# Kernel tuning notes

Measured on AMD Instinct MI355X. Metric: run time of the kernel, lower is better.

The kernel has to match this reference:

```python
import jax, jax.numpy as jnp
import numpy as np

B, N, E, D, L, NC = 48, 96, 1024, 300, 4, 7
NEG = 1e30


def _gru(x, h, w_ih, w_hh, b_ih, b_hh):
    # torch.nn.GRUCell math; weights are (3D, D) in torch layout
    gi = x @ w_ih.T + b_ih
    gh = h @ w_hh.T + b_hh
    ir, iz, inn = jnp.split(gi, 3, axis=-1)
    hr, hz, hn = jnp.split(gh, 3, axis=-1)
    r = jax.nn.sigmoid(ir + hr)
    z = jax.nn.sigmoid(iz + hz)
    n = jnp.tanh(inn + r * hn)
    return (1.0 - z) * n + z * h


def _layer(Cin, Hin, adj, cwi, cwh, cbi, cbh, pwi, pwh, pbi, pbh, wq, wk, gb):
    b, n, d = Cin.shape
    zeros = jnp.zeros((b, d), Cin.dtype)
    c0 = _gru(Cin[:, 0], zeros, cwi, cwh, cbi, cbh)          # GRUCell with h=0
    p0 = _gru(zeros, Cin[:, 0], pwi, pwh, pbi, pbh)          # M=0 at step 0
    P0 = jnp.zeros_like(Cin).at[:, 0].set(p0)                # growing P kept as full buffer
    pos = jnp.arange(n)

    def step(P, i):
        q = Cin[:, i]                                        # (B, D)
        mask = adj[:, i] * (pos < i).astype(adj.dtype)       # only predecessors j < i
        # GatLinear: Linear(cat(Q,K)) == Q.wq + K.wk + b
        alpha = (q @ wq)[:, None] + P @ wk + gb              # (B, N)
        alpha = alpha - (1.0 - mask) * NEG                   # mask_logic
        w = jax.nn.softmax(alpha, axis=-1)
        M = jnp.einsum('bn,bnd->bd', w, P)
        c_i = _gru(q, M, cwi, cwh, cbi, cbh)
        p_i = _gru(M, Hin[:, i], pwi, pwh, pbi, pbh)
        P = jax.lax.dynamic_update_slice(P, p_i[:, None, :], (0, i, 0))
        return P, c_i

    P, Cs = jax.lax.scan(step, P0, jnp.arange(1, n))
    CL = jnp.concatenate([c0[:, None], jnp.moveaxis(Cs, 0, 1)], axis=1)  # (B, N, D)
    return CL, P


def reference(features, adj, s_mask, fc1_w, fc1_b,
              gc_wih, gc_whh, gc_bih, gc_bhh,
              gp_wih, gp_whh, gp_bih, gp_bhh,
              gat_wq, gat_wk, gat_b,
              mlp_w0, mlp_b0, mlp_w1, mlp_b1, mlp_w2, mlp_b2):
    # s_mask is unused when no_rel_attn=True (faithful to torch forward)
    H0 = jax.nn.relu(features @ fc1_w + fc1_b)
    H_list = [H0]
    C_list = [H0]
    for l in range(L):
        CL, P = _layer(C_list[l], H_list[l], adj,
                       gc_wih[l], gc_whh[l], gc_bih[l], gc_bhh[l],
                       gp_wih[l], gp_whh[l], gp_bih[l], gp_bhh[l],
                       gat_wq[l], gat_wk[l], gat_b[l])
        C_list.append(CL)
        H_list.append(CL)
        H_list.append(P)
    H_list.append(features)
    H = jnp.concatenate(H_list, axis=2)                      # (B, N, 9D + E)
    x = jax.nn.relu(H @ mlp_w0 + mlp_b0)
    x = jax.nn.relu(x @ mlp_w1 + mlp_b1)
    logits = x @ mlp_w2 + mlp_b2                             # (B, N, NC)
    return logits


def setup_inputs() -> dict:
    key = jax.random.key(0)
    ks = jax.random.split(key, 25)
    s = 0.02

    def p(k, shape):
        return jax.random.normal(k, shape, jnp.float32) * s

    features = jax.random.normal(ks[0], (B, N, E), jnp.float32)
    # DAG adjacency: random predecessors, strictly lower-triangular, previous
    # utterance always connected (guarantees a nonempty attention context)
    base = jax.random.bernoulli(ks[1], 0.5, (B, N, N)).astype(jnp.float32)
    tri = jnp.tril(jnp.ones((N, N), jnp.float32), -1)
    prev = jnp.eye(N, k=-1, dtype=jnp.float32)
    adj = jnp.maximum(base * tri, prev[None])
    s_mask = jax.random.randint(ks[2], (B, N, N), 0, 2, jnp.int32)
    in_dim = D * (2 * L + 1) + E
    return {
        'features': features, 'adj': adj, 's_mask': s_mask,
        'fc1_w': p(ks[3], (E, D)), 'fc1_b': p(ks[4], (D,)),
        'gc_wih': p(ks[5], (L, 3 * D, D)), 'gc_whh': p(ks[6], (L, 3 * D, D)),
        'gc_bih': p(ks[7], (L, 3 * D)), 'gc_bhh': p(ks[8], (L, 3 * D)),
        'gp_wih': p(ks[9], (L, 3 * D, D)), 'gp_whh': p(ks[10], (L, 3 * D, D)),
        'gp_bih': p(ks[11], (L, 3 * D)), 'gp_bhh': p(ks[12], (L, 3 * D)),
        'gat_wq': p(ks[13], (L, D)), 'gat_wk': p(ks[14], (L, D)), 'gat_b': p(ks[15], (L,)),
        'mlp_w0': p(ks[16], (in_dim, D)), 'mlp_b0': p(ks[17], (D,)),
        'mlp_w1': p(ks[18], (D, D)), 'mlp_b1': p(ks[19], (D,)),
        'mlp_w2': p(ks[20], (D, NC)), 'mlp_b2': p(ks[21], (NC,)),
    }
```

## Files before the change

### kernel.cpp

```cpp
#include <hip/hip_runtime.h>
#include <math.h>

#define BB 48
#define NN 96
#define EE 1024
#define DD 300
#define LL 4
#define G3 900
#define PP 150
#define PP2 152
#define NC4 38
#define HDIM 3724
#define ROWS (BB*NN)
#define NEGI -1.0e30f
#define KP300 304
#define GIC_TILES 540

typedef _Float16 half2_t __attribute__((ext_vector_type(2)));
typedef _Float16 h8 __attribute__((ext_vector_type(8)));
typedef float f4 __attribute__((ext_vector_type(4)));

__device__ __forceinline__ float sigm(float x){ return 1.0f/(1.0f+expf(-x)); }

__device__ __forceinline__ void dot4(const h8 wv, const h8 mc,
                                     float& a0, float& a1, float& a2, float& a3)
{
    half2_t w0,w1,w2,w3,m0,m1,m2,m3;
    w0.x=wv[0]; w0.y=wv[1]; m0.x=mc[0]; m0.y=mc[1];
    w1.x=wv[2]; w1.y=wv[3]; m1.x=mc[2]; m1.y=mc[3];
    w2.x=wv[4]; w2.y=wv[5]; m2.x=mc[4]; m2.y=mc[5];
    w3.x=wv[6]; w3.y=wv[7]; m3.x=mc[6]; m3.y=mc[7];
    a0 = __builtin_amdgcn_fdot2(w0, m0, a0, false);
    a1 = __builtin_amdgcn_fdot2(w1, m1, a1, false);
    a2 = __builtin_amdgcn_fdot2(w2, m2, a2, false);
    a3 = __builtin_amdgcn_fdot2(w3, m3, a3, false);
}

__global__ __launch_bounds__(256) void pack_w_q(const float* __restrict__ src_all,
                                                h8* __restrict__ dst)
{
    int l = blockIdx.y;
    int idx = blockIdx.x*256 + threadIdx.x;
    if (idx >= NC4*G3) return;
    int c = idx / G3, gate = idx % G3;
    const float* src = src_all + (size_t)l*G3*DD + (size_t)gate*DD;
    h8 v;
    #pragma unroll
    for (int j=0;j<8;j++){
        int d = 8*c + j;
        v[j] = (d<DD) ? (_Float16)src[d] : (_Float16)0.f;
    }
    dst[(size_t)l*NC4*G3 + idx] = v;
}

__global__ __launch_bounds__(256) void conv_gru_w(const float* __restrict__ gp_whh,
                                                  const float* __restrict__ gc_wih,
                                                  const float* __restrict__ gc_whh,
                                                  _Float16* __restrict__ outp)
{
    int z = blockIdx.y; int l = z/3, wsel = z%3;
    const float* src = (wsel==0?gp_whh:wsel==1?gc_wih:gc_whh) + (size_t)l*G3*DD;
    _Float16* dst = outp + (size_t)z*G3*KP300;
    int idx = blockIdx.x*256 + threadIdx.x;
    if (idx >= G3*KP300) return;
    int n = idx/KP300, k = idx%KP300;
    dst[idx] = (k<DD) ? (_Float16)src[(size_t)n*DD+k] : (_Float16)0.f;
}

__global__ __launch_bounds__(256) void convT(const float* __restrict__ src,
                                             _Float16* __restrict__ dst,
                                             int K, int N, int Kpad)
{
    int idx = blockIdx.x*256 + threadIdx.x;
    if (idx >= N*Kpad) return;
    int n = idx/Kpad, k = idx%Kpad;
    dst[idx] = (k<K) ? (_Float16)src[(size_t)k*N + n] : (_Float16)0.f;
}

__device__ __forceinline__ void gemm_tile(
    int m0, int n0, int tid,
    const float* __restrict__ A, int lda,
    const _Float16* __restrict__ B, int Kpad,
    const float* __restrict__ bias,
    float* __restrict__ C, int ldc,
    int N, int K, int relu)
{
    constexpr int KPS=40;
    __shared__ _Float16 As[128][KPS];
    __shared__ _Float16 Bs[64][KPS];
    int w = tid>>6, lane = tid&63;
    int wy = w>>1, wx = w&1;
    int lm = lane&15, q = lane>>4;

    f4 acc[4][2];
    #pragma unroll
    for (int a=0;a<4;a++)
        #pragma unroll
        for (int b=0;b<2;b++)
            #pragma unroll
            for (int r=0;r<4;r++) acc[a][b][r]=0.f;

    int am = tid>>1, akg = (tid&1)*16;
    int bn = tid>>2, bkg = (tid&3)*8;
    const float* arow = A + (size_t)(m0+am)*lda;

    for (int k0=0; k0<K; k0+=32){
        {
            __align__(16) _Float16 av[16];
            #pragma unroll
            for (int u=0;u<16;u+=4){
                int k = k0 + akg + u;
                float x0,x1,x2,x3;
                if (k+4 <= K){
                    float4 v = *(const float4*)(arow + k);
                    x0=v.x;x1=v.y;x2=v.z;x3=v.w;
                } else {
                    x0 = (k  <K)? arow[k  ]:0.f;
                    x1 = (k+1<K)? arow[k+1]:0.f;
                    x2 = (k+2<K)? arow[k+2]:0.f;
                    x3 = (k+3<K)? arow[k+3]:0.f;
                }
                av[u]=(_Float16)x0; av[u+1]=(_Float16)x1;
                av[u+2]=(_Float16)x2; av[u+3]=(_Float16)x3;
            }
            *(h8*)&As[am][akg]   = *(h8*)&av[0];
            *(h8*)&As[am][akg+8] = *(h8*)&av[8];
        }
        {
            int gk = k0 + bkg;
            h8 bv;
            #pragma unroll
            for (int j=0;j<8;j++) bv[j]=(_Float16)0.f;
            if (n0+bn < N && gk < Kpad)
                bv = *(const h8*)(B + (size_t)(n0+bn)*Kpad + gk);
            *(h8*)&Bs[bn][bkg] = bv;
        }
        __syncthreads();
        h8 af[4], bf[2];
        #pragma unroll
        for (int mb=0; mb<4; mb++) af[mb] = *(h8*)&As[wy*64+mb*16+lm][q*8];
        #pragma unroll
        for (int nb=0; nb<2; nb++) bf[nb] = *(h8*)&Bs[wx*32+nb*16+lm][q*8];
        #pragma unroll
        for (int mb=0; mb<4; mb++)
            #pragma unroll
            for (int nb=0; nb<2; nb++)
                acc[mb][nb] = __builtin_amdgcn_mfma_f32_16x16x32_f16(af[mb], bf[nb], acc[mb][nb], 0,0,0);
        __syncthreads();
    }
    #pragma unroll
    for (int mb=0; mb<4; mb++){
        int r0 = m0 + wy*64 + mb*16 + q*4;
        #pragma unroll
        for (int nb=0; nb<2; nb++){
            int c = n0 + wx*32 + nb*16 + lm;
            if (c < N){
                float bb = bias[c];
                #pragma unroll
                for (int reg=0; reg<4; reg++){
                    float v = acc[mb][nb][reg] + bb;
                    if (relu) v = fmaxf(v, 0.f);
                    C[(size_t)(r0+reg)*ldc + c] = v;
                }
            }
        }
    }
}

__global__ __launch_bounds__(256) void gemm_mfma(
    const float* __restrict__ A, int lda,
    const _Float16* __restrict__ B, int Kpad,
    const float* __restrict__ bias,
    float* __restrict__ C, int ldc,
    int N, int K, int relu)
{
    gemm_tile(blockIdx.y*128, blockIdx.x*64, threadIdx.x,
              A, lda, B, Kpad, bias, C, ldc, N, K, relu);
}

__global__ void featcopy(const float* __restrict__ f, float* __restrict__ H)
{
    size_t row = blockIdx.x;
    int t = threadIdx.x;
    float4 v = *(const float4*)(f + row*EE + t*4);
    *(float4*)(H + row*HDIM + 2700 + t*4) = v;
}

__global__ __launch_bounds__(1024, 4) void scan_kernel(
    float* __restrict__ Hbuf,
    const float* __restrict__ GHp,
    const h8* __restrict__ pwiQ,
    const h8* __restrict__ pwhQ,
    const float* __restrict__ pbi,
    const float* __restrict__ pbh,
    const float* __restrict__ wk,
    const float* __restrict__ wq,
    const float* __restrict__ gat_b, int lidx,
    const float* __restrict__ adj,
    float* __restrict__ Mbuf,
    int ccol, int hcol, int pcol,
    const _Float16* __restrict__ cwiF,
    const float* __restrict__ cbi,
    float* __restrict__ GIc)
{
    if (blockIdx.x >= BB){
        if (threadIdx.x < 256){
            int bid = blockIdx.x - BB;
            int n0 = (bid % 15)*64, m0 = (bid / 15)*128;
            gemm_tile(m0, n0, threadIdx.x, Hbuf + ccol, HDIM, cwiF, KP300,
                      cbi, GIc, G3, G3, DD, 0);
        }
        return;
    }

    int b = blockIdx.x;
    int t = threadIdx.x;

    __shared__ __align__(16) half2_t P_h2[NN][PP];
    __shared__ __align__(16) float g_s[G3];
    __shared__ __align__(16) float Mpart[3][DD];
    __shared__ __align__(16) half2_t M_h2[PP2];
    __shared__ __align__(16) float e_s[NN];
    __shared__ __align__(16) float pk_s[NN];
    __shared__ __align__(16) float pw_s[DD];
    __shared__ __align__(16) float adj_s[NN*NN];
    __shared__ __align__(16) float qd_s[NN];
    __shared__ __align__(16) float ghp_s[G3];
    __shared__ __align__(16) float hv_s[DD];

    size_t rowbase = (size_t)b*NN;

    h8 wr0,wr1,wr2,wr3,wr4,wr5,wr6,wr7,wr8,wr9,wr10,wr11;
    float pbi_r = 0.f;
    if (t < G3){
        const h8* W = pwiQ + t;
        wr0 = W[0];        wr1 = W[(size_t)1*G3];  wr2 = W[(size_t)2*G3];
        wr3 = W[(size_t)3*G3];  wr4 = W[(size_t)4*G3];  wr5 = W[(size_t)5*G3];
        wr6 = W[(size_t)6*G3];  wr7 = W[(size_t)7*G3];  wr8 = W[(size_t)8*G3];
        wr9 = W[(size_t)9*G3];  wr10 = W[(size_t)10*G3]; wr11 = W[(size_t)11*G3];
        pbi_r = pbi[t];
    }
    float2 wk_r = make_float2(0.f,0.f);
    if (t < PP) wk_r = *(const float2*)&wk[2*t];

    for (int k=t; k<NN*NN; k+=1024) adj_s[k] = adj[rowbase*NN + k];
    {
        int w = t>>6, lane = t&63;
        float gb = gat_b[lidx];
        for (int r = w; r < NN; r += 16){
            const float* x = Hbuf + (rowbase + r)*HDIM + ccol;
            float s = 0.f;
            for (int d=lane; d<DD; d+=64) s += x[d]*wq[d];
            #pragma unroll
            for (int o=32;o>0;o>>=1) s += __shfl_xor(s,o);
            if (lane==0) qd_s[r] = s + gb;
        }
    }
    if (t < PP){
        float2 c2 = *(const float2*)&Hbuf[rowbase*HDIM + ccol + 2*t];
        Mpart[0][2*t] = c2.x; Mpart[0][2*t+1] = c2.y;
        half2_t mh; mh.x = (_Float16)c2.x; mh.y = (_Float16)c2.y;
        M_h2[t] = mh;
    } else if (t < PP2){
        half2_t z; z.x=(_Float16)0.f; z.y=(_Float16)0.f;
        M_h2[t] = z;
    }
    __syncthreads();
    if (t < G3){
        const h8* W = pwhQ + t;
        float a0=0.f, a1=0.f, a2=0.f, a3=0.f;
        #pragma unroll 4
        for (int c=0;c<NC4;c++){
            h8 wv = W[(size_t)c*G3];
            h8 mc = *(h8*)&M_h2[4*c];
            dot4(wv, mc, a0,a1,a2,a3);
        }
        g_s[t] = pbh[t] + (a0+a2) + (a1+a3);
    }
    __syncthreads();
    if (t < PP){
        int d0 = 2*t, d1 = 2*t+1;
        float r0  = sigm(pbi[d0]      + g_s[d0]);
        float z0  = sigm(pbi[DD+d0]   + g_s[DD+d0]);
        float n0  = tanhf(pbi[2*DD+d0] + r0*g_s[2*DD+d0]);
        float p0  = (1.f-z0)*n0 + z0*Mpart[0][d0];
        float r1  = sigm(pbi[d1]      + g_s[d1]);
        float z1  = sigm(pbi[DD+d1]   + g_s[DD+d1]);
        float n1  = tanhf(pbi[2*DD+d1] + r1*g_s[2*DD+d1]);
        float p1  = (1.f-z1)*n1 + z1*Mpart[0][d1];
        *(float2*)&Hbuf[rowbase*HDIM + pcol + d0] = make_float2(p0,p1);
        half2_t ph; ph.x = (_Float16)p0; ph.y = (_Float16)p1;
        P_h2[0][t] = ph;
        pw_s[d0] = p0*wk_r.x;
        pw_s[d1] = p1*wk_r.y;
        *(float2*)&Mbuf[rowbase*DD + d0] = make_float2(0.f,0.f);
    }
    __syncthreads();

    for (int i=1;i<NN;i++){
        size_t row = rowbase + i;
        if (t < 64){
            float s = 0.f;
            for (int c=t;c<DD;c+=64) s += pw_s[c];
            #pragma unroll
            for (int o=32;o>0;o>>=1) s += __shfl_xor(s,o);
            if (t==0) pk_s[i-1] = s;
            float q = qd_s[i];
            float a0 = NEGI, a1 = NEGI;
            if (t < i){
                if (adj_s[i*NN+t] != 0.f) a0 = q + ((t==i-1)? s : pk_s[t]);
            }
            int j1 = 64+t;
            if (t < 32 && j1 < i){
                if (adj_s[i*NN+j1] != 0.f) a1 = q + ((j1==i-1)? s : pk_s[j1]);
            }
            float m = fmaxf(a0,a1);
            #pragma unroll
            for (int o=32;o>0;o>>=1) m = fmaxf(m, __shfl_xor(m,o));
            float e0 = expf(a0-m);
            float e1 = (t<32)? expf(a1-m) : 0.f;
            float ss = e0+e1;
            #pragma unroll
            for (int o=32;o>0;o>>=1) ss += __shfl_xor(ss,o);
            float inv = 1.f/ss;
            e_s[t] = e0*inv;
            if (t<32) e_s[64+t] = e1*inv;
        }
        __syncthreads();
        if (t < 450){
            int g = t/150, dp = t%150;
            int cnt = (i+2)/3;
            int j0 = g*cnt; int j1 = j0+cnt; if (j1 > i) j1 = i;
            float m0=0.f, m1=0.f;
            for (int j=j0;j<j1;j++){
                float w = e_s[j];
                half2_t pv = P_h2[j][dp];
                m0 += w*(float)pv.x;
                m1 += w*(float)pv.y;
            }
            *(float2*)&Mpart[g][2*dp] = make_float2(m0,m1);
        } else if (t >= 512){
            int k = t-512;
            #pragma unroll
            for (int it=0; it<2; it++){
                int idx = k + it*512;
                if (idx < 450){
                    *(float2*)&ghp_s[2*idx] = *(const float2*)&GHp[row*G3 + 2*idx];
                } else if (idx < 600){
                    int h = idx-450;
                    *(float2*)&hv_s[2*h] = *(const float2*)&Hbuf[row*HDIM + hcol + 2*h];
                }
            }
        }
        __syncthreads();
        if (t < PP){
            float m0 = Mpart[0][2*t] + Mpart[1][2*t] + Mpart[2][2*t];
            float m1 = Mpart[0][2*t+1] + Mpart[1][2*t+1] + Mpart[2][2*t+1];
            half2_t mh; mh.x = (_Float16)m0; mh.y = (_Float16)m1;
            M_h2[t] = mh;
            *(float2*)&Mbuf[row*DD + 2*t] = make_float2(m0,m1);
        }
        __syncthreads();
        if (t < G3){
            const h8* W = pwiQ + t;
            float a0=0.f, a1=0.f, a2=0.f, a3=0.f;
            dot4(wr0,  *(h8*)&M_h2[0],  a0,a1,a2,a3);
            dot4(wr1,  *(h8*)&M_h2[4],  a0,a1,a2,a3);
            dot4(wr2,  *(h8*)&M_h2[8],  a0,a1,a2,a3);
            dot4(wr3,  *(h8*)&M_h2[12], a0,a1,a2,a3);
            dot4(wr4,  *(h8*)&M_h2[16], a0,a1,a2,a3);
            dot4(wr5,  *(h8*)&M_h2[20], a0,a1,a2,a3);
            dot4(wr6,  *(h8*)&M_h2[24], a0,a1,a2,a3);
            dot4(wr7,  *(h8*)&M_h2[28], a0,a1,a2,a3);
            dot4(wr8,  *(h8*)&M_h2[32], a0,a1,a2,a3);
            dot4(wr9,  *(h8*)&M_h2[36], a0,a1,a2,a3);
            dot4(wr10, *(h8*)&M_h2[40], a0,a1,a2,a3);
            dot4(wr11, *(h8*)&M_h2[44], a0,a1,a2,a3);
            #pragma unroll 4
            for (int c=12;c<NC4;c++){
                h8 wv = W[(size_t)c*G3];
                h8 mc = *(h8*)&M_h2[4*c];
                dot4(wv, mc, a0,a1,a2,a3);
            }
            g_s[t] = pbi_r + (a0+a2) + (a1+a3);
        }
        __syncthreads();
        if (t < PP){
            int d0 = 2*t, d1 = 2*t+1;
            float2 hv = *(const float2*)&hv_s[d0];
            float r0  = sigm(g_s[d0]      + ghp_s[d0]);
            float z0  = sigm(g_s[DD+d0]   + ghp_s[DD+d0]);
            float n0  = tanhf(g_s[2*DD+d0] + r0*ghp_s[2*DD+d0]);
            float p0  = (1.f-z0)*n0 + z0*hv.x;
            float r1  = sigm(g_s[d1]      + ghp_s[d1]);
            float z1  = sigm(g_s[DD+d1]   + ghp_s[DD+d1]);
            float n1  = tanhf(g_s[2*DD+d1] + r1*ghp_s[2*DD+d1]);
            float p1  = (1.f-z1)*n1 + z1*hv.y;
            *(float2*)&Hbuf[row*HDIM + pcol + d0] = make_float2(p0,p1);
            half2_t ph; ph.x = (_Float16)p0; ph.y = (_Float16)p1;
            P_h2[i][t] = ph;
            pw_s[d0] = p0*wk_r.x;
            pw_s[d1] = p1*wk_r.y;
        }
        __syncthreads();
    }
}

__global__ __launch_bounds__(320) void combine_c(
    const float* __restrict__ GIc, const float* __restrict__ GHc,
    const float* __restrict__ Mbuf, float* __restrict__ Hbuf, int clcol)
{
    size_t row = blockIdx.x;
    int d = threadIdx.x;
    if (d < DD){
        float ir = GIc[row*G3+d], iz = GIc[row*G3+DD+d], inn = GIc[row*G3+2*DD+d];
        float hr = GHc[row*G3+d], hz = GHc[row*G3+DD+d], hn  = GHc[row*G3+2*DD+d];
        float r  = sigm(ir+hr);
        float z  = sigm(iz+hz);
        float nn = tanhf(inn + r*hn);
        float h  = Mbuf[row*DD+d];
        Hbuf[row*HDIM + clcol + d] = (1.f-z)*nn + z*h;
    }
}

__global__ __launch_bounds__(64) void logits_kernel(
    const float* __restrict__ x2, const float* __restrict__ w2,
    const float* __restrict__ b2, float* __restrict__ out)
{
    size_t row = blockIdx.x;
    int lane = threadIdx.x;
    float acc[7]={0,0,0,0,0,0,0};
    for (int d=lane; d<DD; d+=64){
        float x = x2[row*DD+d];
        #pragma unroll
        for (int c=0;c<7;c++) acc[c] += x*w2[d*7+c];
    }
    #pragma unroll
    for (int c=0;c<7;c++){
        float s = acc[c];
        #pragma unroll
        for (int o=32;o>0;o>>=1) s += __shfl_down(s,o);
        if (lane==0) out[row*7+c] = s + b2[c];
    }
}

extern "C" void kernel_launch(void* const* d_in, const int* in_sizes, int n_in,
                              void* d_out, int out_size, void* d_ws, size_t ws_size,
                              hipStream_t stream)
{
    const float* features = (const float*)d_in[0];
    const float* adj      = (const float*)d_in[1];
    const float* fc1_w    = (const float*)d_in[3];
    const float* fc1_b    = (const float*)d_in[4];
    const float* gc_wih   = (const float*)d_in[5];
    const float* gc_whh   = (const float*)d_in[6];
    const float* gc_bih   = (const float*)d_in[7];
    const float* gc_bhh   = (const float*)d_in[8];
    const float* gp_wih   = (const float*)d_in[9];
    const float* gp_whh   = (const float*)d_in[10];
    const float* gp_bih   = (const float*)d_in[11];
    const float* gp_bhh   = (const float*)d_in[12];
    const float* gat_wq   = (const float*)d_in[13];
    const float* gat_wk   = (const float*)d_in[14];
    const float* gat_b    = (const float*)d_in[15];
    const float* mlp_w0   = (const float*)d_in[16];
    const float* mlp_b0   = (const float*)d_in[17];
    const float* mlp_w1   = (const float*)d_in[18];
    const float* mlp_b1   = (const float*)d_in[19];
    const float* mlp_w2   = (const float*)d_in[20];
    const float* mlp_b2   = (const float*)d_in[21];
    float* out = (float*)d_out;

    float* ws = (float*)d_ws;
    size_t off = 0;
    float* Hbuf = ws + off; off += (size_t)ROWS*HDIM;
    float* bufA = ws + off; off += (size_t)ROWS*G3;
    float* bufB = ws + off; off += (size_t)ROWS*G3;
    float* bufC = ws + off; off += (size_t)ROWS*G3;
    float* Mbuf = ws + off; off += (size_t)ROWS*DD;
    h8* pwiQ = (h8*)(ws + off); off += (size_t)LL*NC4*G3*4;
    h8* pwhQ = (h8*)(ws + off); off += (size_t)LL*NC4*G3*4;
    _Float16* gruF = (_Float16*)(ws + off); off += (size_t)12*G3*KP300/2;
    _Float16* fc1F = (_Float16*)(ws + off); off += (size_t)DD*EE/2;
    _Float16* mlp0F= (_Float16*)(ws + off); off += (size_t)DD*3728/2;
    _Float16* mlp1F= (_Float16*)(ws + off); off += (size_t)DD*KP300/2;
    (void)ws_size; (void)in_sizes; (void)n_in; (void)out_size;

    {
        pack_w_q<<<dim3((NC4*G3+255)/256, LL), 256, 0, stream>>>(gp_wih, pwiQ);
        pack_w_q<<<dim3((NC4*G3+255)/256, LL), 256, 0, stream>>>(gp_whh, pwhQ);
        conv_gru_w<<<dim3((G3*KP300+255)/256, 12), 256, 0, stream>>>(gp_whh, gc_wih, gc_whh, gruF);
        convT<<<(DD*EE+255)/256, 256, 0, stream>>>(fc1_w, fc1F, EE, DD, EE);
        convT<<<(DD*3728+255)/256, 256, 0, stream>>>(mlp_w0, mlp0F, HDIM, DD, 3728);
        convT<<<(DD*KP300+255)/256, 256, 0, stream>>>(mlp_w1, mlp1F, DD, DD, KP300);
    }
    gemm_mfma<<<dim3(5,36),256,0,stream>>>(features, EE, fc1F, EE, fc1_b,
                                           Hbuf, HDIM, DD, EE, 1);
    featcopy<<<ROWS,256,0,stream>>>(features, Hbuf);

    for (int l=0;l<LL;l++){
        int ccol  = (l==0)? 0 : 300 + (l-1)*600;
        int hcol  = l*300;
        int pcol  = 600 + l*600;
        int clcol = 300 + l*600;
        const h8* pwiQl = pwiQ + (size_t)l*NC4*G3;
        const h8* pwhQl = pwhQ + (size_t)l*NC4*G3;
        const _Float16* pwhF = gruF + (size_t)(l*3+0)*G3*KP300;
        const _Float16* cwiF = gruF + (size_t)(l*3+1)*G3*KP300;
        const _Float16* cwhF = gruF + (size_t)(l*3+2)*G3*KP300;

        gemm_mfma<<<dim3(15,36),256,0,stream>>>(Hbuf+hcol, HDIM, pwhF, KP300,
                                                gp_bhh + l*G3, bufA, G3, G3, DD, 0);
        scan_kernel<<<BB+GIC_TILES,1024,0,stream>>>(Hbuf, bufA, pwiQl, pwhQl,
                                          gp_bih + l*G3, gp_bhh + l*G3,
                                          gat_wk + l*DD, gat_wq + l*DD, gat_b, l,
                                          adj, Mbuf, ccol, hcol, pcol,
                                          cwiF, gc_bih + l*G3, bufB);
        gemm_mfma<<<dim3(15,36),256,0,stream>>>(Mbuf, DD, cwhF, KP300,
                                                gc_bhh + l*G3, bufC, G3, G3, DD, 0);
        combine_c<<<ROWS,320,0,stream>>>(bufB, bufC, Mbuf, Hbuf, clcol);
    }

    gemm_mfma<<<dim3(5,36),256,0,stream>>>(Hbuf, HDIM, mlp0F, 3728, mlp_b0,
                                           bufB, DD, DD, HDIM, 1);
    gemm_mfma<<<dim3(5,36),256,0,stream>>>(bufB, DD, mlp1F, KP300, mlp_b1,
                                           bufC, DD, DD, DD, 1);
    logits_kernel<<<ROWS,64,0,stream>>>(bufC, mlp_w2, mlp_b2, out);
}
```

Measured before the change: 3.190 ms.

## Precompute W_ih·P rows and mix them by attention weights in the scan

Uses linearity of the GRU input projection: W_ih·M = sum_j w_j (W_ih·P_j). Each step now projects only the newly produced P row (K_j = W_ih P_j), stores it in a global buffer, and forms the input gates as an attention-weighted sum of stored K rows. The per-step weighted M reduction is dropped; attention weights go to a buffer and a separate m_gemm kernel rebuilds M afterwards for the C-branch GRU. Also double-buffers the prefetch of GHp/Hin rows and cuts one barrier per step, at the cost of O(i·900) global reads per step and extra traffic for K and E.

```diff
diff --git a/kernel.cpp b/kernel.cpp
--- a/kernel.cpp
+++ b/kernel.cpp
@@ -8,7 +8,6 @@
 #define LL 4
 #define G3 900
 #define PP 150
-#define PP2 152
 #define NC4 38
 #define HDIM 3724
 #define ROWS (BB*NN)
@@ -197,7 +196,8 @@
     const float* __restrict__ wq,
     const float* __restrict__ gat_b, int lidx,
     const float* __restrict__ adj,
-    float* __restrict__ Mbuf,
+    float* __restrict__ Kf,
+    float* __restrict__ Ebuf,
     int ccol, int hcol, int pcol,
     const _Float16* __restrict__ cwiF,
     const float* __restrict__ cbi,
@@ -216,32 +216,32 @@
     int b = blockIdx.x;
     int t = threadIdx.x;
 
-    __shared__ __align__(16) half2_t P_h2[NN][PP];
+    __shared__ __align__(16) _Float16 P_s[NN][304];
+    __shared__ __align__(16) float adj_s[NN*NN];
     __shared__ __align__(16) float g_s[G3];
-    __shared__ __align__(16) float Mpart[3][DD];
-    __shared__ __align__(16) half2_t M_h2[PP2];
-    __shared__ __align__(16) float e_s[NN];
-    __shared__ __align__(16) float pk_s[NN];
-    __shared__ __align__(16) float pw_s[DD];
-    __shared__ __align__(16) float adj_s[NN*NN];
-    __shared__ __align__(16) float qd_s[NN];
-    __shared__ __align__(16) float ghp_s[G3];
-    __shared__ __align__(16) float hv_s[DD];
+    __shared__ __align__(16) float ghp_s[2][G3];
+    __shared__ __align__(16) float hv_s[2][DD];
+    __shared__ __align__(16) _Float16 cin_h[304];
+    __shared__ float e_s[NN];
+    __shared__ float pk_s[NN];
+    __shared__ float qd_s[NN];
+    __shared__ float pksum[8];
 
     size_t rowbase = (size_t)b*NN;
 
-    h8 wr0,wr1,wr2,wr3,wr4,wr5,wr6,wr7,wr8,wr9,wr10,wr11;
-    float pbi_r = 0.f;
+    h8 wr0,wr1,wr2,wr3,wr4,wr5,wr6,wr7,wr8,wr9,wr10,wr11,wr12,wr13,wr14,wr15;
+    float pbi_r = 0.f, wk_r = 0.f;
     if (t < G3){
         const h8* W = pwiQ + t;
-        wr0 = W[0];        wr1 = W[(size_t)1*G3];  wr2 = W[(size_t)2*G3];
+        wr0 = W[0];             wr1 = W[(size_t)1*G3];  wr2 = W[(size_t)2*G3];
         wr3 = W[(size_t)3*G3];  wr4 = W[(size_t)4*G3];  wr5 = W[(size_t)5*G3];
         wr6 = W[(size_t)6*G3];  wr7 = W[(size_t)7*G3];  wr8 = W[(size_t)8*G3];
         wr9 = W[(size_t)9*G3];  wr10 = W[(size_t)10*G3]; wr11 = W[(size_t)11*G3];
+        wr12 = W[(size_t)12*G3]; wr13 = W[(size_t)13*G3]; wr14 = W[(size_t)14*G3];
+        wr15 = W[(size_t)15*G3];
         pbi_r = pbi[t];
     }
-    float2 wk_r = make_float2(0.f,0.f);
-    if (t < PP) wk_r = *(const float2*)&wk[2*t];
+    if (t < DD) wk_r = wk[t];
 
     for (int k=t; k<NN*NN; k+=1024) adj_s[k] = adj[rowbase*NN + k];
     {
@@ -256,153 +256,173 @@
             if (lane==0) qd_s[r] = s + gb;
         }
     }
-    if (t < PP){
+    if (t < 150){
         float2 c2 = *(const float2*)&Hbuf[rowbase*HDIM + ccol + 2*t];
-        Mpart[0][2*t] = c2.x; Mpart[0][2*t+1] = c2.y;
-        half2_t mh; mh.x = (_Float16)c2.x; mh.y = (_Float16)c2.y;
-        M_h2[t] = mh;
-    } else if (t < PP2){
-        half2_t z; z.x=(_Float16)0.f; z.y=(_Float16)0.f;
-        M_h2[t] = z;
+        cin_h[2*t]   = (_Float16)c2.x;
+        cin_h[2*t+1] = (_Float16)c2.y;
+    } else if (t < 152){
+        cin_h[2*t]   = (_Float16)0.f;
+        cin_h[2*t+1] = (_Float16)0.f;
+    }
+    if (t >= 256 && t < 352) Ebuf[rowbase*NN + (t-256)] = 0.f;
+    if (t >= 512 && t < 812){
+        int idx = t-512; size_t nrow = rowbase+1;
+        if (idx < 225)
+            *(float4*)&ghp_s[1][idx*4] = *(const float4*)&GHp[nrow*G3 + idx*4];
+        else {
+            int hh = idx-225;
+            *(float4*)&hv_s[1][hh*4] = *(const float4*)&Hbuf[nrow*HDIM + hcol + hh*4];
+        }
     }
     __syncthreads();
     if (t < G3){
-        const h8* W = pwhQ + t;
+        const h8* W2 = pwhQ + t;
+        const h8* Cc = (const h8*)cin_h;
         float a0=0.f, a1=0.f, a2=0.f, a3=0.f;
         #pragma unroll 4
-        for (int c=0;c<NC4;c++){
-            h8 wv = W[(size_t)c*G3];
-            h8 mc = *(h8*)&M_h2[4*c];
-            dot4(wv, mc, a0,a1,a2,a3);
-        }
+        for (int c=0;c<NC4;c++) dot4(W2[(size_t)c*G3], Cc[c], a0,a1,a2,a3);
         g_s[t] = pbh[t] + (a0+a2) + (a1+a3);
     }
     __syncthreads();
-    if (t < PP){
-        int d0 = 2*t, d1 = 2*t+1;
-        float r0  = sigm(pbi[d0]      + g_s[d0]);
-        float z0  = sigm(pbi[DD+d0]   + g_s[DD+d0]);
-        float n0  = tanhf(pbi[2*DD+d0] + r0*g_s[2*DD+d0]);
-        float p0  = (1.f-z0)*n0 + z0*Mpart[0][d0];
-        float r1  = sigm(pbi[d1]      + g_s[d1]);
-        float z1  = sigm(pbi[DD+d1]   + g_s[DD+d1]);
-        float n1  = tanhf(pbi[2*DD+d1] + r1*g_s[2*DD+d1]);
-        float p1  = (1.f-z1)*n1 + z1*Mpart[0][d1];
-        *(float2*)&Hbuf[rowbase*HDIM + pcol + d0] = make_float2(p0,p1);
-        half2_t ph; ph.x = (_Float16)p0; ph.y = (_Float16)p1;
-        P_h2[0][t] = ph;
-        pw_s[d0] = p0*wk_r.x;
-        pw_s[d1] = p1*wk_r.y;
-        *(float2*)&Mbuf[rowbase*DD + d0] = make_float2(0.f,0.f);
+    if (t < 320){
+        int d = t; float pw = 0.f;
+        if (d < DD){
+            float cin = Hbuf[rowbase*HDIM + ccol + d];
+            float r = sigm(pbi[d]        + g_s[d]);
+            float z = sigm(pbi[DD+d]     + g_s[DD+d]);
+            float n = tanhf(pbi[2*DD+d]  + r*g_s[2*DD+d]);
+            float p = (1.f-z)*n + z*cin;
+            Hbuf[rowbase*HDIM + pcol + d] = p;
+            P_s[0][d] = (_Float16)p;
+            pw = p * wk_r;
+        } else if (d < 304){
+            P_s[0][d] = (_Float16)0.f;
+        }
+        #pragma unroll
+        for (int o=32;o>0;o>>=1) pw += __shfl_xor(pw,o);
+        if ((t&63)==0) pksum[t>>6] = pw;
     }
     __syncthreads();
 
     for (int i=1;i<NN;i++){
         size_t row = rowbase + i;
-        if (t < 64){
-            float s = 0.f;
-            for (int c=t;c<DD;c+=64) s += pw_s[c];
-            #pragma unroll
-            for (int o=32;o>0;o>>=1) s += __shfl_xor(s,o);
-            if (t==0) pk_s[i-1] = s;
+        if (t < G3){
+            const h8* W  = pwiQ + t;
+            const h8* Pr = (const h8*)&P_s[i-1][0];
+            float a0=0.f, a1=0.f, a2=0.f, a3=0.f;
+            dot4(wr0,  Pr[0],  a0,a1,a2,a3);
+            dot4(wr1,  Pr[1],  a0,a1,a2,a3);
+            dot4(wr2,  Pr[2],  a0,a1,a2,a3);
+            dot4(wr3,  Pr[3],  a0,a1,a2,a3);
+            dot4(wr4,  Pr[4],  a0,a1,a2,a3);
+            dot4(wr5,  Pr[5],  a0,a1,a2,a3);
+            dot4(wr6,  Pr[6],  a0,a1,a2,a3);
+            dot4(wr7,  Pr[7],  a0,a1,a2,a3);
+            dot4(wr8,  Pr[8],  a0,a1,a2,a3);
+            dot4(wr9,  Pr[9],  a0,a1,a2,a3);
+            dot4(wr10, Pr[10], a0,a1,a2,a3);
+            dot4(wr11, Pr[11], a0,a1,a2,a3);
+            dot4(wr12, Pr[12], a0,a1,a2,a3);
+            dot4(wr13, Pr[13], a0,a1,a2,a3);
+            dot4(wr14, Pr[14], a0,a1,a2,a3);
+            dot4(wr15, Pr[15], a0,a1,a2,a3);
+            #pragma unroll 4
+            for (int c=16;c<NC4;c++){
+                dot4(W[(size_t)c*G3], Pr[c], a0,a1,a2,a3);
+            }
+            Kf[(row-1)*G3 + t] = (a0+a2) + (a1+a3);
+        } else if (t >= 960){
+            int lane = t - 960;
+            float s_last = pksum[0]+pksum[1]+pksum[2]+pksum[3]+pksum[4];
+            if (lane==0) pk_s[i-1] = s_last;
             float q = qd_s[i];
             float a0 = NEGI, a1 = NEGI;
-            if (t < i){
-                if (adj_s[i*NN+t] != 0.f) a0 = q + ((t==i-1)? s : pk_s[t]);
-            }
-            int j1 = 64+t;
-            if (t < 32 && j1 < i){
-                if (adj_s[i*NN+j1] != 0.f) a1 = q + ((j1==i-1)? s : pk_s[j1]);
-            }
+            if (lane < i && adj_s[i*NN+lane] != 0.f)
+                a0 = q + ((lane==i-1)? s_last : pk_s[lane]);
+            int j1 = 64+lane;
+            if (lane < 32 && j1 < i && adj_s[i*NN+j1] != 0.f)
+                a1 = q + ((j1==i-1)? s_last : pk_s[j1]);
             float m = fmaxf(a0,a1);
             #pragma unroll
             for (int o=32;o>0;o>>=1) m = fmaxf(m, __shfl_xor(m,o));
             float e0 = expf(a0-m);
-            float e1 = (t<32)? expf(a1-m) : 0.f;
+            float e1 = (lane<32)? expf(a1-m) : 0.f;
             float ss = e0+e1;
             #pragma unroll
             for (int o=32;o>0;o>>=1) ss += __shfl_xor(ss,o);
             float inv = 1.f/ss;
-            e_s[t] = e0*inv;
-            if (t<32) e_s[64+t] = e1*inv;
-        }
-        __syncthreads();
-        if (t < 450){
-            int g = t/150, dp = t%150;
-            int cnt = (i+2)/3;
-            int j0 = g*cnt; int j1 = j0+cnt; if (j1 > i) j1 = i;
-            float m0=0.f, m1=0.f;
-            for (int j=j0;j<j1;j++){
-                float w = e_s[j];
-                half2_t pv = P_h2[j][dp];
-                m0 += w*(float)pv.x;
-                m1 += w*(float)pv.y;
-            }
-            *(float2*)&Mpart[g][2*dp] = make_float2(m0,m1);
-        } else if (t >= 512){
-            int k = t-512;
-            #pragma unroll
-            for (int it=0; it<2; it++){
-                int idx = k + it*512;
-                if (idx < 450){
-                    *(float2*)&ghp_s[2*idx] = *(const float2*)&GHp[row*G3 + 2*idx];
-                } else if (idx < 600){
-                    int h = idx-450;
-                    *(float2*)&hv_s[2*h] = *(const float2*)&Hbuf[row*HDIM + hcol + 2*h];
-                }
-            }
-        }
-        __syncthreads();
-        if (t < PP){
-            float m0 = Mpart[0][2*t] + Mpart[1][2*t] + Mpart[2][2*t];
-            float m1 = Mpart[0][2*t+1] + Mpart[1][2*t+1] + Mpart[2][2*t+1];
-            half2_t mh; mh.x = (_Float16)m0; mh.y = (_Float16)m1;
-            M_h2[t] = mh;
-            *(float2*)&Mbuf[row*DD + 2*t] = make_float2(m0,m1);
+            e_s[lane] = e0*inv;
+            if (lane<32) e_s[64+lane] = e1*inv;
         }
         __syncthreads();
         if (t < G3){
-            const h8* W = pwiQ + t;
-            float a0=0.f, a1=0.f, a2=0.f, a3=0.f;
-            dot4(wr0,  *(h8*)&M_h2[0],  a0,a1,a2,a3);
-            dot4(wr1,  *(h8*)&M_h2[4],  a0,a1,a2,a3);
-            dot4(wr2,  *(h8*)&M_h2[8],  a0,a1,a2,a3);
-            dot4(wr3,  *(h8*)&M_h2[12], a0,a1,a2,a3);
-            dot4(wr4,  *(h8*)&M_h2[16], a0,a1,a2,a3);
-            dot4(wr5,  *(h8*)&M_h2[20], a0,a1,a2,a3);
-            dot4(wr6,  *(h8*)&M_h2[24], a0,a1,a2,a3);
-            dot4(wr7,  *(h8*)&M_h2[28], a0,a1,a2,a3);
-            dot4(wr8,  *(h8*)&M_h2[32], a0,a1,a2,a3);
-            dot4(wr9,  *(h8*)&M_h2[36], a0,a1,a2,a3);
-            dot4(wr10, *(h8*)&M_h2[40], a0,a1,a2,a3);
-            dot4(wr11, *(h8*)&M_h2[44], a0,a1,a2,a3);
+            const float* Kr = Kf + rowbase*G3 + t;
+            float acc = 0.f;
             #pragma unroll 4
-            for (int c=12;c<NC4;c++){
-                h8 wv = W[(size_t)c*G3];
-                h8 mc = *(h8*)&M_h2[4*c];
-                dot4(wv, mc, a0,a1,a2,a3);
+            for (int j=0;j<i;j++)
+                acc = fmaf(e_s[j], Kr[(size_t)j*G3], acc);
+            g_s[t] = acc + pbi_r;
+        } else if (t < 996){
+            Ebuf[row*NN + (t-900)] = e_s[t-900];
+        }
+        __syncthreads();
+        if (t < 320){
+            int d = t; float pw = 0.f;
+            int buf = i&1;
+            if (d < DD){
+                float r = sigm(g_s[d]        + ghp_s[buf][d]);
+                float z = sigm(g_s[DD+d]     + ghp_s[buf][DD+d]);
+                float n = tanhf(g_s[2*DD+d]  + r*ghp_s[buf][2*DD+d]);
+                float p = (1.f-z)*n + z*hv_s[buf][d];
+                Hbuf[row*HDIM + pcol + d] = p;
+                P_s[i][d] = (_Float16)p;
+                pw = p * wk_r;
+            } else if (d < 304){
+                P_s[i][d] = (_Float16)0.f;
             }
-            g_s[t] = pbi_r + (a0+a2) + (a1+a3);
+            #pragma unroll
+            for (int o=32;o>0;o>>=1) pw += __shfl_xor(pw,o);
+            if ((t&63)==0) pksum[t>>6] = pw;
+        } else if (t >= 384 && t < 684 && i < NN-1){
+            int idx = t-384; size_t nrow = row+1;
+            int buf = (i+1)&1;
+            if (idx < 225)
+                *(float4*)&ghp_s[buf][idx*4] = *(const float4*)&GHp[nrow*G3 + idx*4];
+            else {
+                int hh = idx-225;
+                *(float4*)&hv_s[buf][hh*4] = *(const float4*)&Hbuf[nrow*HDIM + hcol + hh*4];
+            }
         }
         __syncthreads();
-        if (t < PP){
-            int d0 = 2*t, d1 = 2*t+1;
-            float2 hv = *(const float2*)&hv_s[d0];
-            float r0  = sigm(g_s[d0]      + ghp_s[d0]);
-            float z0  = sigm(g_s[DD+d0]   + ghp_s[DD+d0]);
-            float n0  = tanhf(g_s[2*DD+d0] + r0*ghp_s[2*DD+d0]);
-            float p0  = (1.f-z0)*n0 + z0*hv.x;
-            float r1  = sigm(g_s[d1]      + ghp_s[d1]);
-            float z1  = sigm(g_s[DD+d1]   + ghp_s[DD+d1]);
-            float n1  = tanhf(g_s[2*DD+d1] + r1*ghp_s[2*DD+d1]);
-            float p1  = (1.f-z1)*n1 + z1*hv.y;
-            *(float2*)&Hbuf[row*HDIM + pcol + d0] = make_float2(p0,p1);
-            half2_t ph; ph.x = (_Float16)p0; ph.y = (_Float16)p1;
-            P_h2[i][t] = ph;
-            pw_s[d0] = p0*wk_r.x;
-            pw_s[d1] = p1*wk_r.y;
-        }
-        __syncthreads();
+    }
+}
+
+__global__ __launch_bounds__(320) void m_gemm(
+    const float* __restrict__ Ebuf, const float* __restrict__ Hbuf,
+    float* __restrict__ Mbuf, int pcol)
+{
+    int b = blockIdx.y, it = blockIdx.x;
+    __shared__ float Es[16][96];
+    int t = threadIdx.x;
+    size_t rowbase = (size_t)b*NN;
+    for (int k=t; k<16*96; k+=320){
+        int r = k/96, j = k%96;
+        Es[r][j] = Ebuf[(rowbase + it*16 + r)*NN + j];
+    }
+    __syncthreads();
+    if (t < DD){
+        float acc[16];
+        #pragma unroll
+        for (int r=0;r<16;r++) acc[r] = 0.f;
+        int jmax = it*16 + 16; if (jmax > NN) jmax = NN;
+        for (int j=0;j<jmax;j++){
+            float p = Hbuf[(rowbase+j)*HDIM + pcol + t];
+            #pragma unroll
+            for (int r=0;r<16;r++) acc[r] = fmaf(Es[r][j], p, acc[r]);
+        }
+        #pragma unroll
+        for (int r=0;r<16;r++)
+            Mbuf[(rowbase + it*16 + r)*DD + t] = acc[r];
     }
 }
 
@@ -484,6 +504,7 @@
     _Float16* fc1F = (_Float16*)(ws + off); off += (size_t)DD*EE/2;
     _Float16* mlp0F= (_Float16*)(ws + off); off += (size_t)DD*3728/2;
     _Float16* mlp1F= (_Float16*)(ws + off); off += (size_t)DD*KP300/2;
+    float* Ebuf = ws + off; off += (size_t)ROWS*NN;
     (void)ws_size; (void)in_sizes; (void)n_in; (void)out_size;
 
     {
@@ -514,8 +535,9 @@
         scan_kernel<<<BB+GIC_TILES,1024,0,stream>>>(Hbuf, bufA, pwiQl, pwhQl,
                                           gp_bih + l*G3, gp_bhh + l*G3,
                                           gat_wk + l*DD, gat_wq + l*DD, gat_b, l,
-                                          adj, Mbuf, ccol, hcol, pcol,
+                                          adj, bufC, Ebuf, ccol, hcol, pcol,
                                           cwiF, gc_bih + l*G3, bufB);
+        m_gemm<<<dim3(6,BB),320,0,stream>>>(Ebuf, Hbuf, Mbuf, pcol);
         gemm_mfma<<<dim3(15,36),256,0,stream>>>(Mbuf, DD, cwhF, KP300,
                                                 gc_bhh + l*G3, bufC, G3, G3, DD, 0);
         combine_c<<<ROWS,320,0,stream>>>(bufB, bufC, Mbuf, Hbuf, clcol);
```

Result: slower. 3.377 ms (+5.9%).
